# Optimization experiments

Measured on AMD Instinct MI355X. Metric: run time of the kernel, lower is better.

The kernel has to match this reference:

```python
import jax, jax.numpy as jnp
import numpy as np

N_CODES = 512
D = 8
BETA = 0.25


def setup_inputs() -> dict:
    key = jax.random.key(0)
    k1, k2 = jax.random.split(key)
    z = jax.random.normal(k1, (8, D, 16, 64, 64), dtype=jnp.float32)
    # torch init: uniform(-1/n_codes, 1/n_codes)
    codebook = jax.random.uniform(
        k2, (N_CODES, D), dtype=jnp.float32,
        minval=-1.0 / N_CODES, maxval=1.0 / N_CODES)
    return {"z": z, "codebook": codebook}


def reference(z, codebook):
    B, Dc, T, H, W = z.shape
    # [B, T, H, W, D] -> [N, D]
    z_flat = jnp.transpose(z, (0, 2, 3, 4, 1)).reshape(-1, Dc)
    z2 = jnp.sum(z_flat * z_flat, axis=1, keepdims=True)          # [N, 1]
    e2 = jnp.sum(codebook * codebook, axis=1)[None, :]            # [1, K]
    ze = z_flat @ codebook.T                                      # [N, K]
    dists = z2 + e2 - 2.0 * ze
    idx = jnp.argmin(dists, axis=1)                               # [N]
    z_q = jnp.transpose(codebook[idx].reshape(B, T, H, W, Dc), (0, 4, 1, 2, 3))
    commit = jnp.mean((jax.lax.stop_gradient(z_q) - z) ** 2)
    codebk = jnp.mean((z_q - jax.lax.stop_gradient(z)) ** 2)
    vq_loss = codebk + BETA * commit
    z_q_st = z + jax.lax.stop_gradient(z_q - z)
    return z_q_st, vq_loss, idx.reshape(B, T, H, W)
```

## Files before the change

kernel.cpp:

```cpp
#include <hip/hip_runtime.h>


#define NPTS      524288
#define KCODES    512
#define DDIM      8
#define CH_STRIDE 65536
#define B_STRIDE  524288
#define BLK       512
#define NWAVES    8
#define NTILES    32
#define CMAX      4
#define FLT_BIG   3.402823466e+38f

typedef short bf8 __attribute__((ext_vector_type(8)));
typedef float f4  __attribute__((ext_vector_type(4)));

__device__ __forceinline__ unsigned short f2bf(float f) {
    unsigned u = __float_as_uint(f);
    unsigned r = u + 0x7fffu + ((u >> 16) & 1u);
    return (unsigned short)(r >> 16);
}
__device__ __forceinline__ float bf2f(unsigned short h) {
    return __uint_as_float(((unsigned)h) << 16);
}

__device__ __forceinline__ float np_sumsq8(const float* x) {
    float p0 = __fmul_rn(x[0], x[0]);
    float p1 = __fmul_rn(x[1], x[1]);
    float p2 = __fmul_rn(x[2], x[2]);
    float p3 = __fmul_rn(x[3], x[3]);
    float p4 = __fmul_rn(x[4], x[4]);
    float p5 = __fmul_rn(x[5], x[5]);
    float p6 = __fmul_rn(x[6], x[6]);
    float p7 = __fmul_rn(x[7], x[7]);
    return __fadd_rn(__fadd_rn(__fadd_rn(p0, p1), __fadd_rn(p2, p3)),
                     __fadd_rn(__fadd_rn(p4, p5), __fadd_rn(p6, p7)));
}

__device__ __forceinline__ float np_dist(const float* __restrict__ cb,
                                         const float* __restrict__ e2f,
                                         int k, const float* zv, float z2) {
    const float* c = cb + (size_t)k * DDIM;
    float ze = 0.0f;
    #pragma unroll
    for (int j = 0; j < DDIM; ++j) ze = __fmaf_rn(zv[j], c[j], ze);
    return __fmaf_rn(-2.0f, ze, __fadd_rn(z2, e2f[k]));
}

__global__ void prep(const float* __restrict__ cb, float* __restrict__ e2f,
                     unsigned short* __restrict__ wsB, float* __restrict__ out_loss) {
    const int tid = blockIdx.x * 256 + threadIdx.x;
    if (tid == 0) *out_loss = 0.0f;
    const int t    = tid >> 6;
    const int lane = tid & 63;
    const int quad = lane >> 4;
    const int colc = lane & 15;
    const int n    = t * 16 + colc;
    float row[DDIM];
    #pragma unroll
    for (int j = 0; j < DDIM; ++j) row[j] = cb[n * DDIM + j];
    const float e2 = np_sumsq8(row);
    if (quad == 3) e2f[n] = e2;

    unsigned short sh[8];
    #pragma unroll
    for (int j = 0; j < 8; ++j) {
        const unsigned short eh = f2bf(row[j]);
        const unsigned short el = f2bf(__fsub_rn(row[j], bf2f(eh)));
        sh[j] = (quad == 1) ? el : eh;
    }
    if (quad == 3) {
        const unsigned short e2h = f2bf(e2);
        const unsigned short e2l = f2bf(__fsub_rn(e2, bf2f(e2h)));
        sh[0] = e2h; sh[1] = e2l;
        #pragma unroll
        for (int j = 2; j < 8; ++j) sh[j] = 0;
    }
    unsigned short* dst = wsB + (size_t)(t * 64 + lane) * 8;
    #pragma unroll
    for (int j = 0; j < 8; ++j) dst[j] = sh[j];
}

__global__ __launch_bounds__(BLK, 4) void vq_main(
    const float* __restrict__ z, const float* __restrict__ cb,
    const float* __restrict__ e2f, const unsigned short* __restrict__ wsB,
    float* __restrict__ out_zq, float* __restrict__ out_loss,
    float* __restrict__ out_idx)
{
    __shared__ unsigned short ldsB[NTILES * 64 * 8];
    __shared__ int            ccnt[BLK];
    __shared__ unsigned short clist[BLK][CMAX];
    __shared__ float          wsum[NWAVES];

    const int tid  = threadIdx.x;
    const int wave = tid >> 6;
    const int lane = tid & 63;
    const int quad = lane >> 4;
    const int col  = lane & 15;

    {
        const uint4* src = (const uint4*)wsB;
        uint4* dst = (uint4*)ldsB;
        #pragma unroll
        for (int q = 0; q < 4; ++q)
            dst[tid + q * BLK] = src[tid + q * BLK];
    }
    ccnt[tid] = 0;

    const int n = blockIdx.x * BLK + tid;
    const int b = n >> 16;
    const int s = n & 65535;
    const float* zp = z + (size_t)b * B_STRIDE + s;
    float zv[DDIM];
    #pragma unroll
    for (int j = 0; j < DDIM; ++j) zv[j] = zp[(size_t)j * CH_STRIDE];
    const float z2 = np_sumsq8(zv);

    float zmax = z2;
    #pragma unroll
    for (int mk = 1; mk <= 32; mk <<= 1) zmax = fmaxf(zmax, __shfl_xor(zmax, mk, 64));
    const float eps = zmax * 6e-7f + 3e-6f;

    unsigned pkz[8];
    #pragma unroll
    for (int j = 0; j < 8; ++j) {
        const unsigned short hh = f2bf(zv[j]);
        const float zh = bf2f(hh);
        const float zl = __fsub_rn(zv[j], zh);
        const unsigned short ah = f2bf(-2.0f * zh);
        const unsigned short al = f2bf(-2.0f * zl);
        pkz[j] = (unsigned)ah | ((unsigned)al << 16);
    }

    bf8 af0, af1, af2, af3;
#define MK_AFRAG(AF, Q)                                                        \
    {                                                                          \
        const int srcl = (Q)*16 + col;                                         \
        _Pragma("unroll")                                                      \
        for (int j = 0; j < 8; ++j) {                                          \
            const unsigned w = (unsigned)__shfl((int)pkz[j], srcl, 64);        \
            const unsigned us = (quad == 2) ? (w >> 16) : (w & 0xFFFFu);       \
            AF[j] = (short)us;                                                 \
        }                                                                      \
        if (quad == 3) AF = (bf8){(short)0x3F80, (short)0x3F80, 0, 0, 0, 0, 0, 0}; \
    }
    MK_AFRAG(af0, 0) MK_AFRAG(af1, 1) MK_AFRAG(af2, 2) MK_AFRAG(af3, 3)

    __syncthreads();

    const bf8* __restrict__ Bp = (const bf8*)ldsB;

    f4 mn0 = (f4){FLT_BIG, FLT_BIG, FLT_BIG, FLT_BIG};
    f4 mn1 = mn0, mn2 = mn0, mn3 = mn0;
    #pragma unroll 4
    for (int t = 0; t < NTILES; ++t) {
        const bf8 bfrag = Bp[t * 64 + lane];
        f4 zero = (f4){0.0f, 0.0f, 0.0f, 0.0f};
        const f4 a0 = __builtin_amdgcn_mfma_f32_16x16x32_bf16(af0, bfrag, zero, 0, 0, 0);
        const f4 a1 = __builtin_amdgcn_mfma_f32_16x16x32_bf16(af1, bfrag, zero, 0, 0, 0);
        const f4 a2 = __builtin_amdgcn_mfma_f32_16x16x32_bf16(af2, bfrag, zero, 0, 0, 0);
        const f4 a3 = __builtin_amdgcn_mfma_f32_16x16x32_bf16(af3, bfrag, zero, 0, 0, 0);
        #pragma unroll
        for (int r = 0; r < 4; ++r) {
            mn0[r] = fminf(mn0[r], a0[r]); mn1[r] = fminf(mn1[r], a1[r]);
            mn2[r] = fminf(mn2[r], a2[r]); mn3[r] = fminf(mn3[r], a3[r]);
        }
    }
    #pragma unroll
    for (int mk = 1; mk <= 8; mk <<= 1) {
        #pragma unroll
        for (int r = 0; r < 4; ++r) {
            mn0[r] = fminf(mn0[r], __shfl_xor(mn0[r], mk, 64));
            mn1[r] = fminf(mn1[r], __shfl_xor(mn1[r], mk, 64));
            mn2[r] = fminf(mn2[r], __shfl_xor(mn2[r], mk, 64));
            mn3[r] = fminf(mn3[r], __shfl_xor(mn3[r], mk, 64));
        }
    }
    #pragma unroll
    for (int r = 0; r < 4; ++r) {
        mn0[r] += eps; mn1[r] += eps; mn2[r] += eps; mn3[r] += eps;
    }

    const int pbase = wave * 64 + quad * 4;
    #pragma unroll 4
    for (int t = 0; t < NTILES; ++t) {
        const bf8 bfrag = Bp[t * 64 + lane];
        f4 zero = (f4){0.0f, 0.0f, 0.0f, 0.0f};
        const f4 a0 = __builtin_amdgcn_mfma_f32_16x16x32_bf16(af0, bfrag, zero, 0, 0, 0);
        const f4 a1 = __builtin_amdgcn_mfma_f32_16x16x32_bf16(af1, bfrag, zero, 0, 0, 0);
        const f4 a2 = __builtin_amdgcn_mfma_f32_16x16x32_bf16(af2, bfrag, zero, 0, 0, 0);
        const f4 a3 = __builtin_amdgcn_mfma_f32_16x16x32_bf16(af3, bfrag, zero, 0, 0, 0);
        const unsigned short code = (unsigned short)(t * 16 + col);
#define PUSH(AQ, MQ, Q)                                                        \
    {                                                                          \
        const bool c0 = AQ[0] <= MQ[0], c1 = AQ[1] <= MQ[1];                   \
        const bool c2 = AQ[2] <= MQ[2], c3 = AQ[3] <= MQ[3];                   \
        if (c0 | c1 | c2 | c3) {                                               \
            const int pt = pbase + (Q)*16;                                     \
            if (c0) { int p = atomicAdd(&ccnt[pt + 0], 1); if (p < CMAX) clist[pt + 0][p] = code; } \
            if (c1) { int p = atomicAdd(&ccnt[pt + 1], 1); if (p < CMAX) clist[pt + 1][p] = code; } \
            if (c2) { int p = atomicAdd(&ccnt[pt + 2], 1); if (p < CMAX) clist[pt + 2][p] = code; } \
            if (c3) { int p = atomicAdd(&ccnt[pt + 3], 1); if (p < CMAX) clist[pt + 3][p] = code; } \
        }                                                                      \
    }
        PUSH(a0, mn0, 0) PUSH(a1, mn1, 1) PUSH(a2, mn2, 2) PUSH(a3, mn3, 3)
    }

    asm volatile("s_waitcnt lgkmcnt(0)" ::: "memory");

    const int cnt = ccnt[tid];
    int bidx;
    if (cnt == 1) {
        bidx = clist[tid][0];
    } else if (cnt <= CMAX) {
        float best = FLT_BIG; bidx = 0;
        for (int i = 0; i < cnt; ++i) {
            const int k = clist[tid][i];
            const float d = np_dist(cb, e2f, k, zv, z2);
            if (d < best || (d == best && k < bidx)) { best = d; bidx = k; }
        }
    } else {
        float best = FLT_BIG; bidx = 0;
        for (int k = 0; k < KCODES; ++k) {
            const float d = np_dist(cb, e2f, k, zv, z2);
            if (d < best) { best = d; bidx = k; }
        }
    }
    out_idx[n] = (float)bidx;

    const float* cw = cb + (size_t)bidx * DDIM;
    float* op = out_zq + (size_t)b * B_STRIDE + s;
    float lsum = 0.0f;
    #pragma unroll
    for (int j = 0; j < DDIM; ++j) {
        const float zq = cw[j];
        const float t  = __fsub_rn(zq, zv[j]);
        op[(size_t)j * CH_STRIDE] = __fadd_rn(zv[j], t);
        lsum = __fmaf_rn(t, t, lsum);
    }

    #pragma unroll
    for (int off = 32; off > 0; off >>= 1) lsum += __shfl_down(lsum, off, 64);
    if (lane == 0) wsum[wave] = lsum;
    __syncthreads();
    if (tid == 0) {
        float bs = 0.0f;
        #pragma unroll
        for (int w = 0; w < NWAVES; ++w) bs += wsum[w];
        atomicAdd(out_loss, bs * (1.25f / 4194304.0f));
    }
}

extern "C" void kernel_launch(void* const* d_in, const int* in_sizes, int n_in,
                              void* d_out, int out_size, void* d_ws, size_t ws_size,
                              hipStream_t stream) {
    const float* z  = (const float*)d_in[0];
    const float* cb = (const float*)d_in[1];
    float* out      = (float*)d_out;
    float* out_zq   = out;
    float* out_loss = out + 4194304;
    float* out_idx  = out + 4194305;
    float* e2f            = (float*)d_ws;
    unsigned short* wsB   = (unsigned short*)((char*)d_ws + 2048);

    prep<<<8, 256, 0, stream>>>(cb, e2f, wsB, out_loss);
    vq_main<<<NPTS / BLK, BLK, 0, stream>>>(z, cb, e2f, wsB,
                                            out_zq, out_loss, out_idx);
}
```

Measured before the change: 120.5 us.

## Read codebook fragments from global memory and spread loss atomics over 64 slots

Drops the per-block copy of the 32 KB bf16 codebook fragments into LDS and the barrier that followed it. The MFMA loop now reads B fragments directly from global memory, relying on L1/L2 caching, which frees LDS and may allow more blocks per CU. The single contended loss atomic is replaced by 64 striped partial sums, reduced and scaled by a small extra finisher kernel. The cost is an extra kernel launch and global-load latency inside the inner loop.

```diff
diff --git a/kernel.cpp b/kernel.cpp
--- a/kernel.cpp
+++ b/kernel.cpp
@@ -10,6 +10,7 @@
 #define NWAVES    8
 #define NTILES    32
 #define CMAX      4
+#define NLOSS     64
 #define FLT_BIG   3.402823466e+38f
 
 typedef short bf8 __attribute__((ext_vector_type(8)));
@@ -48,9 +49,10 @@
 }
 
 __global__ void prep(const float* __restrict__ cb, float* __restrict__ e2f,
-                     unsigned short* __restrict__ wsB, float* __restrict__ out_loss) {
+                     unsigned short* __restrict__ wsB,
+                     float* __restrict__ loss_ws) {
     const int tid = blockIdx.x * 256 + threadIdx.x;
-    if (tid == 0) *out_loss = 0.0f;
+    if (tid < NLOSS) loss_ws[tid] = 0.0f;
     const int t    = tid >> 6;
     const int lane = tid & 63;
     const int quad = lane >> 4;
@@ -84,10 +86,9 @@
 __global__ __launch_bounds__(BLK, 4) void vq_main(
     const float* __restrict__ z, const float* __restrict__ cb,
     const float* __restrict__ e2f, const unsigned short* __restrict__ wsB,
-    float* __restrict__ out_zq, float* __restrict__ out_loss,
+    float* __restrict__ out_zq, float* __restrict__ loss_ws,
     float* __restrict__ out_idx)
 {
-    __shared__ unsigned short ldsB[NTILES * 64 * 8];
     __shared__ int            ccnt[BLK];
     __shared__ unsigned short clist[BLK][CMAX];
     __shared__ float          wsum[NWAVES];
@@ -98,13 +99,6 @@
     const int quad = lane >> 4;
     const int col  = lane & 15;
 
-    {
-        const uint4* src = (const uint4*)wsB;
-        uint4* dst = (uint4*)ldsB;
-        #pragma unroll
-        for (int q = 0; q < 4; ++q)
-            dst[tid + q * BLK] = src[tid + q * BLK];
-    }
     ccnt[tid] = 0;
 
     const int n = blockIdx.x * BLK + tid;
@@ -146,9 +140,7 @@
     }
     MK_AFRAG(af0, 0) MK_AFRAG(af1, 1) MK_AFRAG(af2, 2) MK_AFRAG(af3, 3)
 
-    __syncthreads();
-
-    const bf8* __restrict__ Bp = (const bf8*)ldsB;
+    const bf8* __restrict__ Bp = (const bf8*)wsB;
 
     f4 mn0 = (f4){FLT_BIG, FLT_BIG, FLT_BIG, FLT_BIG};
     f4 mn1 = mn0, mn2 = mn0, mn3 = mn0;
@@ -247,8 +239,17 @@
         float bs = 0.0f;
         #pragma unroll
         for (int w = 0; w < NWAVES; ++w) bs += wsum[w];
-        atomicAdd(out_loss, bs * (1.25f / 4194304.0f));
-    }
+        atomicAdd(&loss_ws[blockIdx.x & (NLOSS - 1)], bs);
+    }
+}
+
+__global__ void loss_fin(const float* __restrict__ loss_ws,
+                         float* __restrict__ out_loss) {
+    const int lane = threadIdx.x;
+    float v = loss_ws[lane];
+    #pragma unroll
+    for (int off = 32; off > 0; off >>= 1) v += __shfl_down(v, off, 64);
+    if (lane == 0) *out_loss = v * (1.25f / 4194304.0f);
 }
 
 extern "C" void kernel_launch(void* const* d_in, const int* in_sizes, int n_in,
@@ -262,8 +263,10 @@
     float* out_idx  = out + 4194305;
     float* e2f            = (float*)d_ws;
     unsigned short* wsB   = (unsigned short*)((char*)d_ws + 2048);
-
-    prep<<<8, 256, 0, stream>>>(cb, e2f, wsB, out_loss);
+    float* loss_ws        = (float*)((char*)d_ws + 2048 + 32768);
+
+    prep<<<8, 256, 0, stream>>>(cb, e2f, wsB, loss_ws);
     vq_main<<<NPTS / BLK, BLK, 0, stream>>>(z, cb, e2f, wsB,
-                                            out_zq, out_loss, out_idx);
-}
+                                            out_zq, loss_ws, out_idx);
+    loss_fin<<<1, 64, 0, stream>>>(loss_ws, out_loss);
+}
```

Result: slower. 123.7 us (+2.7%).
